# Performance work log

Hardware: AMD Instinct MI355X
Metric: run time of the kernel (lower is better)

## Reference

```python
import jax, jax.numpy as jnp
import numpy as np

N = 4096
C_IN = 256
C_OUT = 256
HEADS = 4
C_HEAD = C_OUT // HEADS
ALPHA = 0.2
NEG_FILL = -9e15


def setup_inputs() -> dict:
    key = jax.random.key(0)
    k1, k2, k3, k4 = jax.random.split(key, 4)
    node_feats = jax.random.normal(k1, (N, C_IN), dtype=jnp.float32)
    adj_matrix = jax.random.randint(k2, (1, N, N), 0, 2, dtype=jnp.int32)
    # xavier_uniform with gain=1.414
    lim_w = 1.414 * np.sqrt(6.0 / (C_IN + C_OUT))
    W = jax.random.uniform(k3, (C_OUT, C_IN), minval=-lim_w, maxval=lim_w, dtype=jnp.float32)
    b = jnp.zeros((C_OUT,), dtype=jnp.float32)
    lim_a = 1.414 * np.sqrt(6.0 / (HEADS + 2 * C_HEAD))
    a = jax.random.uniform(k4, (HEADS, 2 * C_HEAD), minval=-lim_a, maxval=lim_a, dtype=jnp.float32)
    return {"node_feats": node_feats, "adj_matrix": adj_matrix, "W": W, "b": b, "a": a}


def reference(node_feats, adj_matrix, W, b, a):
    # node_feats: [N, c_in] -> batch of 1, as in the torch 2D path
    h = (node_feats @ W.T + b).reshape(1, N, HEADS, C_HEAD)  # [1,N,H,c]
    a_src, a_dst = a[:, :C_HEAD], a[:, C_HEAD:]
    # attn logit for edge (i, j) = leakyrelu(a . [h_i, h_j])
    e_src = jnp.einsum('bnhc,hc->bnh', h, a_src)  # contribution of row node i
    e_dst = jnp.einsum('bnhc,hc->bnh', h, a_dst)  # contribution of col node j
    logits = jax.nn.leaky_relu(e_src[:, :, None, :] + e_dst[:, None, :, :], ALPHA)  # [1,N,N,H]
    mask = (adj_matrix == 1)[..., None]  # [1,N,N,1]
    attn = jnp.where(mask, logits, jnp.float32(NEG_FILL))
    probs = jax.nn.softmax(attn, axis=2)  # softmax over neighbors j
    out = jnp.einsum('bijh,bjhc->bihc', probs, h)  # [1,N,H,c]
    return out.reshape(1, N, HEADS * C_HEAD)  # concat heads
```

## Files before the change

kernel.cpp:

```cpp
#include <hip/hip_runtime.h>
#include <hip/hip_bf16.h>


#define NN 4096
#define LOG2E 1.4426950408889634f

typedef float f32x4 __attribute__((ext_vector_type(4)));
typedef int i32x4 __attribute__((ext_vector_type(4)));
typedef unsigned int u32x2 __attribute__((ext_vector_type(2)));
typedef unsigned int u32x4 __attribute__((ext_vector_type(4)));
typedef unsigned short u16x4 __attribute__((ext_vector_type(4)));
typedef unsigned short u16x8 __attribute__((ext_vector_type(8)));
typedef __bf16 bf16x8 __attribute__((ext_vector_type(8)));

__device__ __forceinline__ unsigned short f2bf_rne(float f) {
    unsigned int u = __builtin_bit_cast(unsigned int, f);
    u += 0x7fffu + ((u >> 16) & 1u);
    return (unsigned short)(u >> 16);
}

__device__ __forceinline__ bf16x8 ld_cvt8(const float* __restrict__ p) {
    f32x4 x = *(const f32x4*)p;
    f32x4 y = *(const f32x4*)(p + 4);
    u16x8 u;
    u[0] = f2bf_rne(x[0]); u[1] = f2bf_rne(x[1]); u[2] = f2bf_rne(x[2]); u[3] = f2bf_rne(x[3]);
    u[4] = f2bf_rne(y[0]); u[5] = f2bf_rne(y[1]); u[6] = f2bf_rne(y[2]); u[7] = f2bf_rne(y[3]);
    return __builtin_bit_cast(bf16x8, u);
}

__global__ __launch_bounds__(256) void k1_fused(const float* __restrict__ X,
                                                const float* __restrict__ W,
                                                const float* __restrict__ bias,
                                                const float* __restrict__ a,
                                                unsigned short* __restrict__ hB,
                                                float* __restrict__ esrc,
                                                float* __restrict__ edst) {
    const int lane = threadIdx.x & 63;
    const int hh   = threadIdx.x >> 6;
    const int row  = lane & 15;
    const int kg   = lane >> 4;
    const int rowbase = blockIdx.x * 16;

    f32x4 acc[4];
#pragma unroll
    for (int n = 0; n < 4; ++n) acc[n] = (f32x4)0.f;

#pragma unroll
    for (int kk = 0; kk < 8; ++kk) {
        const int kb = kk * 32 + kg * 8;
        bf16x8 a0 = ld_cvt8(X + (rowbase + row) * 256 + kb);
#pragma unroll
        for (int n = 0; n < 4; ++n) {
            bf16x8 bb = ld_cvt8(W + (hh * 64 + n * 16 + row) * 256 + kb);
            acc[n] = __builtin_amdgcn_mfma_f32_16x16x32_bf16(a0, bb, acc[n], 0, 0, 0);
        }
    }

    const int t   = rowbase >> 5;
    const int lp  = (((rowbase >> 4) & 1) * 2 + (kg >> 1)) * 16 + row;
    const int eoff = (kg & 1) * 4;
    unsigned short* hbb = hB + (hh * 128 + t) * 2048 + lp * 8 + eoff;

    float eS0 = 0.f, eS1 = 0.f, eS2 = 0.f, eS3 = 0.f;
    float eT0 = 0.f, eT1 = 0.f, eT2 = 0.f, eT3 = 0.f;
#pragma unroll
    for (int n = 0; n < 4; ++n) {
        const int col = hh * 64 + n * 16 + row;
        const float bv = bias[col];
        f32x4 hv;
        hv[0] = acc[n][0] + bv; hv[1] = acc[n][1] + bv;
        hv[2] = acc[n][2] + bv; hv[3] = acc[n][3] + bv;
        u16x4 us;
        us[0] = f2bf_rne(hv[0]); us[1] = f2bf_rne(hv[1]);
        us[2] = f2bf_rne(hv[2]); us[3] = f2bf_rne(hv[3]);
        *(u16x4*)(hbb + n * 512) = us;
        const float as_ = a[hh * 128 + n * 16 + row];
        const float ad_ = a[hh * 128 + 64 + n * 16 + row];
        eS0 += hv[0] * as_; eS1 += hv[1] * as_; eS2 += hv[2] * as_; eS3 += hv[3] * as_;
        eT0 += hv[0] * ad_; eT1 += hv[1] * ad_; eT2 += hv[2] * ad_; eT3 += hv[3] * ad_;
    }
#pragma unroll
    for (int d = 1; d < 16; d <<= 1) {
        eS0 += __shfl_xor(eS0, d); eS1 += __shfl_xor(eS1, d);
        eS2 += __shfl_xor(eS2, d); eS3 += __shfl_xor(eS3, d);
        eT0 += __shfl_xor(eT0, d); eT1 += __shfl_xor(eT1, d);
        eT2 += __shfl_xor(eT2, d); eT3 += __shfl_xor(eT3, d);
    }
    if (row == 0) {
        const int rb = hh * NN + rowbase + kg * 4;
        esrc[rb + 0] = eS0 * LOG2E; esrc[rb + 1] = eS1 * LOG2E;
        esrc[rb + 2] = eS2 * LOG2E; esrc[rb + 3] = eS3 * LOG2E;
        edst[rb + 0] = eT0 * LOG2E; edst[rb + 1] = eT1 * LOG2E;
        edst[rb + 2] = eT2 * LOG2E; edst[rb + 3] = eT3 * LOG2E;
    }
}

#define K3_MKP(AF, ES, M8) {                                                      \
    f32x4 s0v = E0 + (f32x4)(ES);                                                 \
    f32x4 s1v = E1 + (f32x4)(ES);                                                 \
    s0v = __builtin_elementwise_max(s0v, s0v * 0.2f);                             \
    s1v = __builtin_elementwise_max(s1v, s1v * 0.2f);                             \
    bf16x8 afv;                                                                   \
    afv[0] = (__bf16)__builtin_exp2f(s0v[0]);                                     \
    afv[1] = (__bf16)__builtin_exp2f(s0v[1]);                                     \
    afv[2] = (__bf16)__builtin_exp2f(s0v[2]);                                     \
    afv[3] = (__bf16)__builtin_exp2f(s0v[3]);                                     \
    afv[4] = (__bf16)__builtin_exp2f(s1v[0]);                                     \
    afv[5] = (__bf16)__builtin_exp2f(s1v[1]);                                     \
    afv[6] = (__bf16)__builtin_exp2f(s1v[2]);                                     \
    afv[7] = (__bf16)__builtin_exp2f(s1v[3]);                                     \
    u32x4 aw = __builtin_bit_cast(u32x4, afv);                                    \
    const u32x2 mk0 = mlut[(M8) & 15u];                                           \
    const u32x2 mk1 = mlut[((M8) >> 4) & 15u];                                    \
    aw[0] &= mk0[0]; aw[1] &= mk0[1];                                             \
    aw[2] &= mk1[0]; aw[3] &= mk1[1];                                             \
    AF = __builtin_bit_cast(bf16x8, aw);                                          \
}

__global__ __launch_bounds__(512, 4) void k3_flash(const int* __restrict__ adj,
                                                   const unsigned short* __restrict__ hB,
                                                   const float* __restrict__ esrc,
                                                   const float* __restrict__ edst,
                                                   float* __restrict__ out) {
    __shared__ float lacc[8][16][64];
    __shared__ float lls[8][16];
    __shared__ u32x2 mlut[16];

    const int lane = threadIdx.x & 63;
    const int q  = threadIdx.x >> 6;
    const int hh = blockIdx.x & 3;
    const int ib = blockIdx.x >> 2;
    const int i0 = ib * 32;
    const int row = lane & 15;
    const int kg  = lane >> 4;

    if (threadIdx.x < 16) {
        const unsigned n = threadIdx.x;
        u32x2 m;
        m[0] = ((n & 1u) ? 0xFFFFu : 0u) | ((n & 2u) ? 0xFFFF0000u : 0u);
        m[1] = ((n & 4u) ? 0xFFFFu : 0u) | ((n & 8u) ? 0xFFFF0000u : 0u);
        mlut[n] = m;
    }
    __syncthreads();

    const float es0 = esrc[hh * NN + i0 + row];
    const float es1 = esrc[hh * NN + i0 + 16 + row];
    const int* adj0 = adj + (i0 + row) * NN + q * 512 + kg * 8;
    const int* adj1 = adj0 + 16 * NN;
    const float* eD = edst + hh * NN + q * 512 + kg * 8;
    const unsigned short* hBp = hB + ((hh * 128 + q * 16) * 256 + lane) * 8;

    u16x8 ou;
    const unsigned short ov = (row == 0) ? (unsigned short)0x3F80 : (unsigned short)0;
#pragma unroll
    for (int e = 0; e < 8; ++e) ou[e] = ov;
    const bf16x8 bOnes = __builtin_bit_cast(bf16x8, ou);

    f32x4 aA0 = (f32x4)0.f, aA1 = (f32x4)0.f, aA2 = (f32x4)0.f,
          aA3 = (f32x4)0.f, aA4 = (f32x4)0.f;
    f32x4 aB0 = (f32x4)0.f, aB1 = (f32x4)0.f, aB2 = (f32x4)0.f,
          aB3 = (f32x4)0.f, aB4 = (f32x4)0.f;

    for (int td = 0; td < 4; ++td) {
        unsigned w0 = 0, w1 = 0;
#pragma unroll
        for (int ti = 0; ti < 4; ++ti) {
            const i32x4 pa0 = *(const i32x4*)(adj0 + td * 128 + ti * 32);
            const i32x4 pa1 = *(const i32x4*)(adj0 + td * 128 + ti * 32 + 4);
            const i32x4 pb0 = *(const i32x4*)(adj1 + td * 128 + ti * 32);
            const i32x4 pb1 = *(const i32x4*)(adj1 + td * 128 + ti * 32 + 4);
            unsigned b0 = 0, b1 = 0;
#pragma unroll
            for (int e = 0; e < 4; ++e) {
                b0 |= (unsigned)(pa0[e] & 1) << e;
                b0 |= (unsigned)(pa1[e] & 1) << (4 + e);
                b1 |= (unsigned)(pb0[e] & 1) << e;
                b1 |= (unsigned)(pb1[e] & 1) << (4 + e);
            }
            w0 |= b0 << (ti * 8);
            w1 |= b1 << (ti * 8);
        }

        const float* eDt = eD + td * 128;
        const unsigned short* hBt = hBp + td * 8192;
#pragma unroll
        for (int ti = 0; ti < 4; ++ti) {
            const f32x4 E0 = *(const f32x4*)(eDt + ti * 32);
            const f32x4 E1 = *(const f32x4*)(eDt + ti * 32 + 4);
            const u16x8 B0 = *(const u16x8*)(hBt + ti * 2048);
            const u16x8 B1 = *(const u16x8*)(hBt + ti * 2048 + 512);
            const u16x8 B2 = *(const u16x8*)(hBt + ti * 2048 + 1024);
            const u16x8 B3 = *(const u16x8*)(hBt + ti * 2048 + 1536);
            bf16x8 af0, af1;
            K3_MKP(af0, es0, (w0 >> (ti * 8)))
            K3_MKP(af1, es1, (w1 >> (ti * 8)))
            aA0 = __builtin_amdgcn_mfma_f32_16x16x32_bf16(af0, __builtin_bit_cast(bf16x8, B0), aA0, 0, 0, 0);
            aA1 = __builtin_amdgcn_mfma_f32_16x16x32_bf16(af0, __builtin_bit_cast(bf16x8, B1), aA1, 0, 0, 0);
            aA2 = __builtin_amdgcn_mfma_f32_16x16x32_bf16(af0, __builtin_bit_cast(bf16x8, B2), aA2, 0, 0, 0);
            aA3 = __builtin_amdgcn_mfma_f32_16x16x32_bf16(af0, __builtin_bit_cast(bf16x8, B3), aA3, 0, 0, 0);
            aA4 = __builtin_amdgcn_mfma_f32_16x16x32_bf16(af0, bOnes, aA4, 0, 0, 0);
            aB0 = __builtin_amdgcn_mfma_f32_16x16x32_bf16(af1, __builtin_bit_cast(bf16x8, B0), aB0, 0, 0, 0);
            aB1 = __builtin_amdgcn_mfma_f32_16x16x32_bf16(af1, __builtin_bit_cast(bf16x8, B1), aB1, 0, 0, 0);
            aB2 = __builtin_amdgcn_mfma_f32_16x16x32_bf16(af1, __builtin_bit_cast(bf16x8, B2), aB2, 0, 0, 0);
            aB3 = __builtin_amdgcn_mfma_f32_16x16x32_bf16(af1, __builtin_bit_cast(bf16x8, B3), aB3, 0, 0, 0);
            aB4 = __builtin_amdgcn_mfma_f32_16x16x32_bf16(af1, bOnes, aB4, 0, 0, 0);
        }
    }

#pragma unroll
    for (int n = 0; n < 4; ++n) {
        f32x4 an = (n == 0) ? aA0 : (n == 1) ? aA1 : (n == 2) ? aA2 : aA3;
#pragma unroll
        for (int r = 0; r < 4; ++r)
            lacc[q][kg * 4 + r][n * 16 + row] = an[r];
    }
    if (row == 0) {
#pragma unroll
        for (int r = 0; r < 4; ++r) lls[q][kg * 4 + r] = aA4[r];
    }
    __syncthreads();
    if (threadIdx.x < 256) {
        const int idx = threadIdx.x * 4;
        const int r2 = idx >> 6;
        const int c  = idx & 63;
        f32x4 v = (f32x4)0.f;
        float l = 0.f;
#pragma unroll
        for (int q2 = 0; q2 < 8; ++q2) {
            v += *(const f32x4*)&lacc[q2][r2][c];
            l += lls[q2][r2];
        }
        const float inv = 1.f / l;
        f32x4 o;
        o[0] = v[0] * inv; o[1] = v[1] * inv; o[2] = v[2] * inv; o[3] = v[3] * inv;
        *(f32x4*)(out + (i0 + r2) * 256 + hh * 64 + c) = o;
    }
    __syncthreads();

#pragma unroll
    for (int n = 0; n < 4; ++n) {
        f32x4 an = (n == 0) ? aB0 : (n == 1) ? aB1 : (n == 2) ? aB2 : aB3;
#pragma unroll
        for (int r = 0; r < 4; ++r)
            lacc[q][kg * 4 + r][n * 16 + row] = an[r];
    }
    if (row == 0) {
#pragma unroll
        for (int r = 0; r < 4; ++r) lls[q][kg * 4 + r] = aB4[r];
    }
    __syncthreads();
    if (threadIdx.x < 256) {
        const int idx = threadIdx.x * 4;
        const int r2 = idx >> 6;
        const int c  = idx & 63;
        f32x4 v = (f32x4)0.f;
        float l = 0.f;
#pragma unroll
        for (int q2 = 0; q2 < 8; ++q2) {
            v += *(const f32x4*)&lacc[q2][r2][c];
            l += lls[q2][r2];
        }
        const float inv = 1.f / l;
        f32x4 o;
        o[0] = v[0] * inv; o[1] = v[1] * inv; o[2] = v[2] * inv; o[3] = v[3] * inv;
        *(f32x4*)(out + (i0 + 16 + r2) * 256 + hh * 64 + c) = o;
    }
}

extern "C" void kernel_launch(void* const* d_in, const int* in_sizes, int n_in,
                              void* d_out, int out_size, void* d_ws, size_t ws_size,
                              hipStream_t stream) {
    const float* X    = (const float*)d_in[0];
    const int*   adj  = (const int*)d_in[1];
    const float* W    = (const float*)d_in[2];
    const float* bias = (const float*)d_in[3];
    const float* a    = (const float*)d_in[4];
    float* out = (float*)d_out;

    char* ws = (char*)d_ws;
    unsigned short* hB   = (unsigned short*)(ws);
    float*          esrc = (float*)(ws + (2 << 20));
    float*          edst = (float*)(ws + (2 << 20) + (64 << 10));

    k1_fused<<<256, 256, 0, stream>>>(X, W, bias, a, hB, esrc, edst);
    k3_flash<<<512, 512, 0, stream>>>(adj, hB, esrc, edst, out);
}
```

Measured before the change: 68.12 us.

## Stream adjacency through LDS with async triple-buffered loads and retile work split

The attention kernel now stages the int32 adjacency rows into shared memory with global_load_lds in a three-deep ring, waiting on vmcnt so the loads overlap the exp/MFMA work. The work split also changes: each block takes 64 rows of one head, each wave owns 16 rows and half the neighbor range, and the grid halves to 256 blocks. The final reduction is simpler because only two waves per row group are combined. In exchange, LDS use grows by 96 KB per block and occupancy is lowered to 2 blocks per CU, and each wave reuses its B fragments for only one row tile instead of two.

Result: faster. 66.34 us (-2.6%).

```diff
diff --git a/kernel.cpp b/kernel.cpp
--- a/kernel.cpp
+++ b/kernel.cpp
@@ -100,16 +100,15 @@
     f32x4 s1v = E1 + (f32x4)(ES);                                                 \
     s0v = __builtin_elementwise_max(s0v, s0v * 0.2f);                             \
     s1v = __builtin_elementwise_max(s1v, s1v * 0.2f);                             \
-    bf16x8 afv;                                                                   \
-    afv[0] = (__bf16)__builtin_exp2f(s0v[0]);                                     \
-    afv[1] = (__bf16)__builtin_exp2f(s0v[1]);                                     \
-    afv[2] = (__bf16)__builtin_exp2f(s0v[2]);                                     \
-    afv[3] = (__bf16)__builtin_exp2f(s0v[3]);                                     \
-    afv[4] = (__bf16)__builtin_exp2f(s1v[0]);                                     \
-    afv[5] = (__bf16)__builtin_exp2f(s1v[1]);                                     \
-    afv[6] = (__bf16)__builtin_exp2f(s1v[2]);                                     \
-    afv[7] = (__bf16)__builtin_exp2f(s1v[3]);                                     \
-    u32x4 aw = __builtin_bit_cast(u32x4, afv);                                    \
+    AF[0] = (__bf16)__builtin_exp2f(s0v[0]);                                      \
+    AF[1] = (__bf16)__builtin_exp2f(s0v[1]);                                      \
+    AF[2] = (__bf16)__builtin_exp2f(s0v[2]);                                      \
+    AF[3] = (__bf16)__builtin_exp2f(s0v[3]);                                      \
+    AF[4] = (__bf16)__builtin_exp2f(s1v[0]);                                      \
+    AF[5] = (__bf16)__builtin_exp2f(s1v[1]);                                      \
+    AF[6] = (__bf16)__builtin_exp2f(s1v[2]);                                      \
+    AF[7] = (__bf16)__builtin_exp2f(s1v[3]);                                      \
+    u32x4 aw = __builtin_bit_cast(u32x4, AF);                                     \
     const u32x2 mk0 = mlut[(M8) & 15u];                                           \
     const u32x2 mk1 = mlut[((M8) >> 4) & 15u];                                    \
     aw[0] &= mk0[0]; aw[1] &= mk0[1];                                             \
@@ -117,22 +116,64 @@
     AF = __builtin_bit_cast(bf16x8, aw);                                          \
 }
 
-__global__ __launch_bounds__(512, 4) void k3_flash(const int* __restrict__ adj,
+#define K3_STAGE(IT, BUF) {                                                       \
+    _Pragma("unroll")                                                             \
+    for (int k = 0; k < 4; ++k)                                                   \
+        __builtin_amdgcn_global_load_lds(                                         \
+            (const __attribute__((address_space(1))) void*)(gbase + (size_t)k * 16384 + (IT) * 64), \
+            (__attribute__((address_space(3))) void*)(&abuf[w][BUF][4 * k][0]),   \
+            16, 0, 0);                                                            \
+}
+
+#define K3_BODY(IT, BUF) {                                                        \
+    const unsigned int* ab = &abuf[w][BUF][0][0];                                 \
+    _Pragma("unroll")                                                             \
+    for (int lt = 0; lt < 2; ++lt) {                                              \
+        const int tl = (IT) * 2 + lt;                                             \
+        const int iloc = (lt * 32 + kg8) ^ rsw;                                   \
+        const u32x4 v0 = *(const u32x4*)(ab + row * 64 + iloc);                   \
+        const u32x4 v1 = *(const u32x4*)(ab + row * 64 + iloc + 4);               \
+        const f32x4 E0 = *(const f32x4*)(eD + tl * 32);                           \
+        const f32x4 E1 = *(const f32x4*)(eD + tl * 32 + 4);                       \
+        const u16x8 B0 = *(const u16x8*)(hBp + tl * 2048);                        \
+        const u16x8 B1 = *(const u16x8*)(hBp + tl * 2048 + 512);                  \
+        const u16x8 B2 = *(const u16x8*)(hBp + tl * 2048 + 1024);                 \
+        const u16x8 B3 = *(const u16x8*)(hBp + tl * 2048 + 1536);                 \
+        unsigned m8 = (v0[0] & 1u)        | ((v0[1] & 1u) << 1)                   \
+                    | ((v0[2] & 1u) << 2) | ((v0[3] & 1u) << 3)                   \
+                    | ((v1[0] & 1u) << 4) | ((v1[1] & 1u) << 5)                   \
+                    | ((v1[2] & 1u) << 6) | ((v1[3] & 1u) << 7);                  \
+        bf16x8 af;                                                                \
+        K3_MKP(af, es0, m8)                                                       \
+        a0 = __builtin_amdgcn_mfma_f32_16x16x32_bf16(af, __builtin_bit_cast(bf16x8, B0), a0, 0, 0, 0); \
+        a1 = __builtin_amdgcn_mfma_f32_16x16x32_bf16(af, __builtin_bit_cast(bf16x8, B1), a1, 0, 0, 0); \
+        a2 = __builtin_amdgcn_mfma_f32_16x16x32_bf16(af, __builtin_bit_cast(bf16x8, B2), a2, 0, 0, 0); \
+        a3 = __builtin_amdgcn_mfma_f32_16x16x32_bf16(af, __builtin_bit_cast(bf16x8, B3), a3, 0, 0, 0); \
+        a4 = __builtin_amdgcn_mfma_f32_16x16x32_bf16(af, bOnes, a4, 0, 0, 0);     \
+    }                                                                             \
+}
+
+__global__ __launch_bounds__(512, 2) void k3_flash(const int* __restrict__ adj,
                                                    const unsigned short* __restrict__ hB,
                                                    const float* __restrict__ esrc,
                                                    const float* __restrict__ edst,
                                                    float* __restrict__ out) {
+    __shared__ unsigned int abuf[8][3][16][64];
     __shared__ float lacc[8][16][64];
     __shared__ float lls[8][16];
     __shared__ u32x2 mlut[16];
 
     const int lane = threadIdx.x & 63;
-    const int q  = threadIdx.x >> 6;
-    const int hh = blockIdx.x & 3;
-    const int ib = blockIdx.x >> 2;
-    const int i0 = ib * 32;
+    const int w  = threadIdx.x >> 6;
+    const int rg = w >> 1;
+    const int jh = w & 1;
+    const int hh = blockIdx.x >> 6;
+    const int ib = blockIdx.x & 63;
+    const int i0 = ib * 64;
     const int row = lane & 15;
     const int kg  = lane >> 4;
+    const int kg8 = kg * 8;
+    const int rsw = (row & 3) << 3;
 
     if (threadIdx.x < 16) {
         const unsigned n = threadIdx.x;
@@ -143,12 +184,14 @@
     }
     __syncthreads();
 
-    const float es0 = esrc[hh * NN + i0 + row];
-    const float es1 = esrc[hh * NN + i0 + 16 + row];
-    const int* adj0 = adj + (i0 + row) * NN + q * 512 + kg * 8;
-    const int* adj1 = adj0 + 16 * NN;
-    const float* eD = edst + hh * NN + q * 512 + kg * 8;
-    const unsigned short* hBp = hB + ((hh * 128 + q * 16) * 256 + lane) * 8;
+    const int lr4  = lane >> 4;
+    const int gloc = (4 * (lane & 15)) ^ (lr4 << 3);
+    const unsigned int* gbase = (const unsigned int*)adj
+        + (size_t)(i0 + rg * 16 + lr4) * NN + jh * 2048 + gloc;
+
+    const float es0 = esrc[hh * NN + i0 + rg * 16 + row];
+    const float* eD = edst + hh * NN + jh * 2048 + kg8;
+    const unsigned short* hBp = hB + (size_t)((hh * 128 + jh * 64) * 256 + lane) * 8;
 
     u16x8 ou;
     const unsigned short ov = (row == 0) ? (unsigned short)0x3F80 : (unsigned short)0;
@@ -156,114 +199,54 @@
     for (int e = 0; e < 8; ++e) ou[e] = ov;
     const bf16x8 bOnes = __builtin_bit_cast(bf16x8, ou);
 
-    f32x4 aA0 = (f32x4)0.f, aA1 = (f32x4)0.f, aA2 = (f32x4)0.f,
-          aA3 = (f32x4)0.f, aA4 = (f32x4)0.f;
-    f32x4 aB0 = (f32x4)0.f, aB1 = (f32x4)0.f, aB2 = (f32x4)0.f,
-          aB3 = (f32x4)0.f, aB4 = (f32x4)0.f;
-
-    for (int td = 0; td < 4; ++td) {
-        unsigned w0 = 0, w1 = 0;
-#pragma unroll
-        for (int ti = 0; ti < 4; ++ti) {
-            const i32x4 pa0 = *(const i32x4*)(adj0 + td * 128 + ti * 32);
-            const i32x4 pa1 = *(const i32x4*)(adj0 + td * 128 + ti * 32 + 4);
-            const i32x4 pb0 = *(const i32x4*)(adj1 + td * 128 + ti * 32);
-            const i32x4 pb1 = *(const i32x4*)(adj1 + td * 128 + ti * 32 + 4);
-            unsigned b0 = 0, b1 = 0;
-#pragma unroll
-            for (int e = 0; e < 4; ++e) {
-                b0 |= (unsigned)(pa0[e] & 1) << e;
-                b0 |= (unsigned)(pa1[e] & 1) << (4 + e);
-                b1 |= (unsigned)(pb0[e] & 1) << e;
-                b1 |= (unsigned)(pb1[e] & 1) << (4 + e);
-            }
-            w0 |= b0 << (ti * 8);
-            w1 |= b1 << (ti * 8);
+    f32x4 a0 = (f32x4)0.f, a1 = (f32x4)0.f, a2 = (f32x4)0.f,
+          a3 = (f32x4)0.f, a4 = (f32x4)0.f;
+
+    K3_STAGE(0, 0)
+    K3_STAGE(1, 1)
+    for (int it = 0; it < 31; ++it) {
+        asm volatile("s_waitcnt vmcnt(4)" ::: "memory");
+        __builtin_amdgcn_sched_barrier(0);
+        const int bf = it % 3;
+        K3_BODY(it, bf)
+        if (it < 30) {
+            const int sb = (it + 2) % 3;
+            K3_STAGE(it + 2, sb)
         }
-
-        const float* eDt = eD + td * 128;
-        const unsigned short* hBt = hBp + td * 8192;
-#pragma unroll
-        for (int ti = 0; ti < 4; ++ti) {
-            const f32x4 E0 = *(const f32x4*)(eDt + ti * 32);
-            const f32x4 E1 = *(const f32x4*)(eDt + ti * 32 + 4);
-            const u16x8 B0 = *(const u16x8*)(hBt + ti * 2048);
-            const u16x8 B1 = *(const u16x8*)(hBt + ti * 2048 + 512);
-            const u16x8 B2 = *(const u16x8*)(hBt + ti * 2048 + 1024);
-            const u16x8 B3 = *(const u16x8*)(hBt + ti * 2048 + 1536);
-            bf16x8 af0, af1;
-            K3_MKP(af0, es0, (w0 >> (ti * 8)))
-            K3_MKP(af1, es1, (w1 >> (ti * 8)))
-            aA0 = __builtin_amdgcn_mfma_f32_16x16x32_bf16(af0, __builtin_bit_cast(bf16x8, B0), aA0, 0, 0, 0);
-            aA1 = __builtin_amdgcn_mfma_f32_16x16x32_bf16(af0, __builtin_bit_cast(bf16x8, B1), aA1, 0, 0, 0);
-            aA2 = __builtin_amdgcn_mfma_f32_16x16x32_bf16(af0, __builtin_bit_cast(bf16x8, B2), aA2, 0, 0, 0);
-            aA3 = __builtin_amdgcn_mfma_f32_16x16x32_bf16(af0, __builtin_bit_cast(bf16x8, B3), aA3, 0, 0, 0);
-            aA4 = __builtin_amdgcn_mfma_f32_16x16x32_bf16(af0, bOnes, aA4, 0, 0, 0);
-            aB0 = __builtin_amdgcn_mfma_f32_16x16x32_bf16(af1, __builtin_bit_cast(bf16x8, B0), aB0, 0, 0, 0);
-            aB1 = __builtin_amdgcn_mfma_f32_16x16x32_bf16(af1, __builtin_bit_cast(bf16x8, B1), aB1, 0, 0, 0);
-            aB2 = __builtin_amdgcn_mfma_f32_16x16x32_bf16(af1, __builtin_bit_cast(bf16x8, B2), aB2, 0, 0, 0);
-            aB3 = __builtin_amdgcn_mfma_f32_16x16x32_bf16(af1, __builtin_bit_cast(bf16x8, B3), aB3, 0, 0, 0);
-            aB4 = __builtin_amdgcn_mfma_f32_16x16x32_bf16(af1, bOnes, aB4, 0, 0, 0);
-        }
-    }
+    }
+    asm volatile("s_waitcnt vmcnt(0)" ::: "memory");
+    __builtin_amdgcn_sched_barrier(0);
+    K3_BODY(31, 1)
 
 #pragma unroll
     for (int n = 0; n < 4; ++n) {
-        f32x4 an = (n == 0) ? aA0 : (n == 1) ? aA1 : (n == 2) ? aA2 : aA3;
+        f32x4 an = (n == 0) ? a0 : (n == 1) ? a1 : (n == 2) ? a2 : a3;
 #pragma unroll
         for (int r = 0; r < 4; ++r)
-            lacc[q][kg * 4 + r][n * 16 + row] = an[r];
+            lacc[w][kg * 4 + r][n * 16 + row] = an[r];
     }
     if (row == 0) {
 #pragma unroll
-        for (int r = 0; r < 4; ++r) lls[q][kg * 4 + r] = aA4[r];
+        for (int r = 0; r < 4; ++r) lls[w][kg * 4 + r] = a4[r];
     }
     __syncthreads();
-    if (threadIdx.x < 256) {
-        const int idx = threadIdx.x * 4;
-        const int r2 = idx >> 6;
-        const int c  = idx & 63;
-        f32x4 v = (f32x4)0.f;
-        float l = 0.f;
-#pragma unroll
-        for (int q2 = 0; q2 < 8; ++q2) {
-            v += *(const f32x4*)&lacc[q2][r2][c];
-            l += lls[q2][r2];
-        }
-        const float inv = 1.f / l;
-        f32x4 o;
-        o[0] = v[0] * inv; o[1] = v[1] * inv; o[2] = v[2] * inv; o[3] = v[3] * inv;
-        *(f32x4*)(out + (i0 + r2) * 256 + hh * 64 + c) = o;
-    }
-    __syncthreads();
-
-#pragma unroll
-    for (int n = 0; n < 4; ++n) {
-        f32x4 an = (n == 0) ? aB0 : (n == 1) ? aB1 : (n == 2) ? aB2 : aB3;
-#pragma unroll
-        for (int r = 0; r < 4; ++r)
-            lacc[q][kg * 4 + r][n * 16 + row] = an[r];
-    }
-    if (row == 0) {
-#pragma unroll
-        for (int r = 0; r < 4; ++r) lls[q][kg * 4 + r] = aB4[r];
-    }
-    __syncthreads();
-    if (threadIdx.x < 256) {
-        const int idx = threadIdx.x * 4;
-        const int r2 = idx >> 6;
-        const int c  = idx & 63;
-        f32x4 v = (f32x4)0.f;
-        float l = 0.f;
-#pragma unroll
-        for (int q2 = 0; q2 < 8; ++q2) {
-            v += *(const f32x4*)&lacc[q2][r2][c];
-            l += lls[q2][r2];
-        }
-        const float inv = 1.f / l;
-        f32x4 o;
-        o[0] = v[0] * inv; o[1] = v[1] * inv; o[2] = v[2] * inv; o[3] = v[3] * inv;
-        *(f32x4*)(out + (i0 + 16 + r2) * 256 + hh * 64 + c) = o;
+
+    {
+        const int rg2 = threadIdx.x >> 7;
+        const int r2  = (threadIdx.x >> 3) & 15;
+        const int c8  = (threadIdx.x & 7) * 8;
+        const int wA = rg2 * 2, wB = rg2 * 2 + 1;
+        f32x4 v0 = *(const f32x4*)&lacc[wA][r2][c8];
+        f32x4 v1 = *(const f32x4*)&lacc[wA][r2][c8 + 4];
+        v0 += *(const f32x4*)&lacc[wB][r2][c8];
+        v1 += *(const f32x4*)&lacc[wB][r2][c8 + 4];
+        const float inv = 1.f / (lls[wA][r2] + lls[wB][r2]);
+        f32x4 o0, o1;
+        o0[0] = v0[0] * inv; o0[1] = v0[1] * inv; o0[2] = v0[2] * inv; o0[3] = v0[3] * inv;
+        o1[0] = v1[0] * inv; o1[1] = v1[1] * inv; o1[2] = v1[2] * inv; o1[3] = v1[3] * inv;
+        float* op = out + (size_t)(i0 + rg2 * 16 + r2) * 256 + hh * 64 + c8;
+        *(f32x4*)op = o0;
+        *(f32x4*)(op + 4) = o1;
     }
 }
 
@@ -283,5 +266,5 @@
     float*          edst = (float*)(ws + (2 << 20) + (64 << 10));
 
     k1_fused<<<256, 256, 0, stream>>>(X, W, bias, a, hB, esrc, edst);
-    k3_flash<<<512, 512, 0, stream>>>(adj, hB, esrc, edst, out);
-}
+    k3_flash<<<256, 512, 0, stream>>>(adj, hB, esrc, edst, out);
+}
```

## Process all heads per block to read adjacency once, with nontemporal prefetch

Applied to the files above, without the earlier changes.

Each block now handles 16 rows across all four heads instead of 32 rows for one head. The adjacency mask is therefore read once per row rather than once per head, which removes the dominant redundant traffic of the 64MB int32 matrix. Adjacency loads are nontemporal and prefetched one tile ahead. In exchange the block count drops to 256 and each thread holds 20 accumulators, with launch bounds relaxed to 2 blocks per CU. This raises register pressure and lowers occupancy, and the epilogue now runs four reduction rounds with barriers.

Result: slower. 72.98 us, median of 2 (+7.1%).

```diff
diff --git a/kernel.cpp b/kernel.cpp
--- a/kernel.cpp
+++ b/kernel.cpp
@@ -95,29 +95,7 @@
     }
 }
 
-#define K3_MKP(AF, ES, M8) {                                                      \
-    f32x4 s0v = E0 + (f32x4)(ES);                                                 \
-    f32x4 s1v = E1 + (f32x4)(ES);                                                 \
-    s0v = __builtin_elementwise_max(s0v, s0v * 0.2f);                             \
-    s1v = __builtin_elementwise_max(s1v, s1v * 0.2f);                             \
-    bf16x8 afv;                                                                   \
-    afv[0] = (__bf16)__builtin_exp2f(s0v[0]);                                     \
-    afv[1] = (__bf16)__builtin_exp2f(s0v[1]);                                     \
-    afv[2] = (__bf16)__builtin_exp2f(s0v[2]);                                     \
-    afv[3] = (__bf16)__builtin_exp2f(s0v[3]);                                     \
-    afv[4] = (__bf16)__builtin_exp2f(s1v[0]);                                     \
-    afv[5] = (__bf16)__builtin_exp2f(s1v[1]);                                     \
-    afv[6] = (__bf16)__builtin_exp2f(s1v[2]);                                     \
-    afv[7] = (__bf16)__builtin_exp2f(s1v[3]);                                     \
-    u32x4 aw = __builtin_bit_cast(u32x4, afv);                                    \
-    const u32x2 mk0 = mlut[(M8) & 15u];                                           \
-    const u32x2 mk1 = mlut[((M8) >> 4) & 15u];                                    \
-    aw[0] &= mk0[0]; aw[1] &= mk0[1];                                             \
-    aw[2] &= mk1[0]; aw[3] &= mk1[1];                                             \
-    AF = __builtin_bit_cast(bf16x8, aw);                                          \
-}
-
-__global__ __launch_bounds__(512, 4) void k3_flash(const int* __restrict__ adj,
+__global__ __launch_bounds__(512, 2) void k3_fused(const int* __restrict__ adj,
                                                    const unsigned short* __restrict__ hB,
                                                    const float* __restrict__ esrc,
                                                    const float* __restrict__ edst,
@@ -128,11 +106,10 @@
 
     const int lane = threadIdx.x & 63;
     const int q  = threadIdx.x >> 6;
-    const int hh = blockIdx.x & 3;
-    const int ib = blockIdx.x >> 2;
-    const int i0 = ib * 32;
+    const int i0 = blockIdx.x * 16;
     const int row = lane & 15;
     const int kg  = lane >> 4;
+    const int kg8 = kg * 8;
 
     if (threadIdx.x < 16) {
         const unsigned n = threadIdx.x;
@@ -143,12 +120,19 @@
     }
     __syncthreads();
 
-    const float es0 = esrc[hh * NN + i0 + row];
-    const float es1 = esrc[hh * NN + i0 + 16 + row];
-    const int* adj0 = adj + (i0 + row) * NN + q * 512 + kg * 8;
-    const int* adj1 = adj0 + 16 * NN;
-    const float* eD = edst + hh * NN + q * 512 + kg * 8;
-    const unsigned short* hBp = hB + ((hh * 128 + q * 16) * 256 + lane) * 8;
+    float es[4];
+#pragma unroll
+    for (int h = 0; h < 4; ++h) es[h] = esrc[h * NN + i0 + row];
+
+    const unsigned int* adjp = (const unsigned int*)adj
+        + (size_t)(i0 + row) * NN + q * 512 + kg8;
+    const float* eD[4];
+    const unsigned short* hBp[4];
+#pragma unroll
+    for (int h = 0; h < 4; ++h) {
+        eD[h]  = edst + h * NN + q * 512 + kg8;
+        hBp[h] = hB + (size_t)((h * 128 + q * 16) * 256 + lane) * 8;
+    }
 
     u16x8 ou;
     const unsigned short ov = (row == 0) ? (unsigned short)0x3F80 : (unsigned short)0;
@@ -156,114 +140,92 @@
     for (int e = 0; e < 8; ++e) ou[e] = ov;
     const bf16x8 bOnes = __builtin_bit_cast(bf16x8, ou);
 
-    f32x4 aA0 = (f32x4)0.f, aA1 = (f32x4)0.f, aA2 = (f32x4)0.f,
-          aA3 = (f32x4)0.f, aA4 = (f32x4)0.f;
-    f32x4 aB0 = (f32x4)0.f, aB1 = (f32x4)0.f, aB2 = (f32x4)0.f,
-          aB3 = (f32x4)0.f, aB4 = (f32x4)0.f;
-
-    for (int td = 0; td < 4; ++td) {
-        unsigned w0 = 0, w1 = 0;
-#pragma unroll
-        for (int ti = 0; ti < 4; ++ti) {
-            const i32x4 pa0 = *(const i32x4*)(adj0 + td * 128 + ti * 32);
-            const i32x4 pa1 = *(const i32x4*)(adj0 + td * 128 + ti * 32 + 4);
-            const i32x4 pb0 = *(const i32x4*)(adj1 + td * 128 + ti * 32);
-            const i32x4 pb1 = *(const i32x4*)(adj1 + td * 128 + ti * 32 + 4);
-            unsigned b0 = 0, b1 = 0;
-#pragma unroll
-            for (int e = 0; e < 4; ++e) {
-                b0 |= (unsigned)(pa0[e] & 1) << e;
-                b0 |= (unsigned)(pa1[e] & 1) << (4 + e);
-                b1 |= (unsigned)(pb0[e] & 1) << e;
-                b1 |= (unsigned)(pb1[e] & 1) << (4 + e);
+    f32x4 acc[4][5];
+#pragma unroll
+    for (int h = 0; h < 4; ++h)
+#pragma unroll
+        for (int n = 0; n < 5; ++n) acc[h][n] = (f32x4)0.f;
+
+    u32x4 c0 = __builtin_nontemporal_load((const u32x4*)(adjp));
+    u32x4 c1 = __builtin_nontemporal_load((const u32x4*)(adjp + 4));
+
+    for (int tl = 0; tl < 16; ++tl) {
+        u32x4 n0, n1;
+        if (tl < 15) {
+            n0 = __builtin_nontemporal_load((const u32x4*)(adjp + (tl + 1) * 32));
+            n1 = __builtin_nontemporal_load((const u32x4*)(adjp + (tl + 1) * 32 + 4));
+        }
+        const unsigned m8 = (c0[0] & 1u)        | ((c0[1] & 1u) << 1)
+                          | ((c0[2] & 1u) << 2) | ((c0[3] & 1u) << 3)
+                          | ((c1[0] & 1u) << 4) | ((c1[1] & 1u) << 5)
+                          | ((c1[2] & 1u) << 6) | ((c1[3] & 1u) << 7);
+        const u32x2 mk0 = mlut[m8 & 15u];
+        const u32x2 mk1 = mlut[(m8 >> 4) & 15u];
+
+#pragma unroll
+        for (int h = 0; h < 4; ++h) {
+            const f32x4 E0 = *(const f32x4*)(eD[h] + tl * 32);
+            const f32x4 E1 = *(const f32x4*)(eD[h] + tl * 32 + 4);
+            const u16x8 B0 = *(const u16x8*)(hBp[h] + tl * 2048);
+            const u16x8 B1 = *(const u16x8*)(hBp[h] + tl * 2048 + 512);
+            const u16x8 B2 = *(const u16x8*)(hBp[h] + tl * 2048 + 1024);
+            const u16x8 B3 = *(const u16x8*)(hBp[h] + tl * 2048 + 1536);
+            f32x4 s0v = E0 + (f32x4)(es[h]);
+            f32x4 s1v = E1 + (f32x4)(es[h]);
+            s0v = __builtin_elementwise_max(s0v, s0v * 0.2f);
+            s1v = __builtin_elementwise_max(s1v, s1v * 0.2f);
+            bf16x8 af;
+            af[0] = (__bf16)__builtin_exp2f(s0v[0]);
+            af[1] = (__bf16)__builtin_exp2f(s0v[1]);
+            af[2] = (__bf16)__builtin_exp2f(s0v[2]);
+            af[3] = (__bf16)__builtin_exp2f(s0v[3]);
+            af[4] = (__bf16)__builtin_exp2f(s1v[0]);
+            af[5] = (__bf16)__builtin_exp2f(s1v[1]);
+            af[6] = (__bf16)__builtin_exp2f(s1v[2]);
+            af[7] = (__bf16)__builtin_exp2f(s1v[3]);
+            u32x4 aw = __builtin_bit_cast(u32x4, af);
+            aw[0] &= mk0[0]; aw[1] &= mk0[1];
+            aw[2] &= mk1[0]; aw[3] &= mk1[1];
+            af = __builtin_bit_cast(bf16x8, aw);
+            acc[h][0] = __builtin_amdgcn_mfma_f32_16x16x32_bf16(af, __builtin_bit_cast(bf16x8, B0), acc[h][0], 0, 0, 0);
+            acc[h][1] = __builtin_amdgcn_mfma_f32_16x16x32_bf16(af, __builtin_bit_cast(bf16x8, B1), acc[h][1], 0, 0, 0);
+            acc[h][2] = __builtin_amdgcn_mfma_f32_16x16x32_bf16(af, __builtin_bit_cast(bf16x8, B2), acc[h][2], 0, 0, 0);
+            acc[h][3] = __builtin_amdgcn_mfma_f32_16x16x32_bf16(af, __builtin_bit_cast(bf16x8, B3), acc[h][3], 0, 0, 0);
+            acc[h][4] = __builtin_amdgcn_mfma_f32_16x16x32_bf16(af, bOnes, acc[h][4], 0, 0, 0);
+        }
+        c0 = n0; c1 = n1;
+    }
+
+#pragma unroll
+    for (int h = 0; h < 4; ++h) {
+#pragma unroll
+        for (int n = 0; n < 4; ++n) {
+#pragma unroll
+            for (int r = 0; r < 4; ++r)
+                lacc[q][kg * 4 + r][n * 16 + row] = acc[h][n][r];
+        }
+        if (row == 0) {
+#pragma unroll
+            for (int r = 0; r < 4; ++r) lls[q][kg * 4 + r] = acc[h][4][r];
+        }
+        __syncthreads();
+        if (threadIdx.x < 256) {
+            const int idx = threadIdx.x * 4;
+            const int r2 = idx >> 6;
+            const int c  = idx & 63;
+            f32x4 v = (f32x4)0.f;
+            float l = 0.f;
+#pragma unroll
+            for (int q2 = 0; q2 < 8; ++q2) {
+                v += *(const f32x4*)&lacc[q2][r2][c];
+                l += lls[q2][r2];
             }
-            w0 |= b0 << (ti * 8);
-            w1 |= b1 << (ti * 8);
-        }
-
-        const float* eDt = eD + td * 128;
-        const unsigned short* hBt = hBp + td * 8192;
-#pragma unroll
-        for (int ti = 0; ti < 4; ++ti) {
-            const f32x4 E0 = *(const f32x4*)(eDt + ti * 32);
-            const f32x4 E1 = *(const f32x4*)(eDt + ti * 32 + 4);
-            const u16x8 B0 = *(const u16x8*)(hBt + ti * 2048);
-            const u16x8 B1 = *(const u16x8*)(hBt + ti * 2048 + 512);
-            const u16x8 B2 = *(const u16x8*)(hBt + ti * 2048 + 1024);
-            const u16x8 B3 = *(const u16x8*)(hBt + ti * 2048 + 1536);
-            bf16x8 af0, af1;
-            K3_MKP(af0, es0, (w0 >> (ti * 8)))
-            K3_MKP(af1, es1, (w1 >> (ti * 8)))
-            aA0 = __builtin_amdgcn_mfma_f32_16x16x32_bf16(af0, __builtin_bit_cast(bf16x8, B0), aA0, 0, 0, 0);
-            aA1 = __builtin_amdgcn_mfma_f32_16x16x32_bf16(af0, __builtin_bit_cast(bf16x8, B1), aA1, 0, 0, 0);
-            aA2 = __builtin_amdgcn_mfma_f32_16x16x32_bf16(af0, __builtin_bit_cast(bf16x8, B2), aA2, 0, 0, 0);
-            aA3 = __builtin_amdgcn_mfma_f32_16x16x32_bf16(af0, __builtin_bit_cast(bf16x8, B3), aA3, 0, 0, 0);
-            aA4 = __builtin_amdgcn_mfma_f32_16x16x32_bf16(af0, bOnes, aA4, 0, 0, 0);
-            aB0 = __builtin_amdgcn_mfma_f32_16x16x32_bf16(af1, __builtin_bit_cast(bf16x8, B0), aB0, 0, 0, 0);
-            aB1 = __builtin_amdgcn_mfma_f32_16x16x32_bf16(af1, __builtin_bit_cast(bf16x8, B1), aB1, 0, 0, 0);
-            aB2 = __builtin_amdgcn_mfma_f32_16x16x32_bf16(af1, __builtin_bit_cast(bf16x8, B2), aB2, 0, 0, 0);
-            aB3 = __builtin_amdgcn_mfma_f32_16x16x32_bf16(af1, __builtin_bit_cast(bf16x8, B3), aB3, 0, 0, 0);
-            aB4 = __builtin_amdgcn_mfma_f32_16x16x32_bf16(af1, bOnes, aB4, 0, 0, 0);
-        }
-    }
-
-#pragma unroll
-    for (int n = 0; n < 4; ++n) {
-        f32x4 an = (n == 0) ? aA0 : (n == 1) ? aA1 : (n == 2) ? aA2 : aA3;
-#pragma unroll
-        for (int r = 0; r < 4; ++r)
-            lacc[q][kg * 4 + r][n * 16 + row] = an[r];
-    }
-    if (row == 0) {
-#pragma unroll
-        for (int r = 0; r < 4; ++r) lls[q][kg * 4 + r] = aA4[r];
-    }
-    __syncthreads();
-    if (threadIdx.x < 256) {
-        const int idx = threadIdx.x * 4;
-        const int r2 = idx >> 6;
-        const int c  = idx & 63;
-        f32x4 v = (f32x4)0.f;
-        float l = 0.f;
-#pragma unroll
-        for (int q2 = 0; q2 < 8; ++q2) {
-            v += *(const f32x4*)&lacc[q2][r2][c];
-            l += lls[q2][r2];
-        }
-        const float inv = 1.f / l;
-        f32x4 o;
-        o[0] = v[0] * inv; o[1] = v[1] * inv; o[2] = v[2] * inv; o[3] = v[3] * inv;
-        *(f32x4*)(out + (i0 + r2) * 256 + hh * 64 + c) = o;
-    }
-    __syncthreads();
-
-#pragma unroll
-    for (int n = 0; n < 4; ++n) {
-        f32x4 an = (n == 0) ? aB0 : (n == 1) ? aB1 : (n == 2) ? aB2 : aB3;
-#pragma unroll
-        for (int r = 0; r < 4; ++r)
-            lacc[q][kg * 4 + r][n * 16 + row] = an[r];
-    }
-    if (row == 0) {
-#pragma unroll
-        for (int r = 0; r < 4; ++r) lls[q][kg * 4 + r] = aB4[r];
-    }
-    __syncthreads();
-    if (threadIdx.x < 256) {
-        const int idx = threadIdx.x * 4;
-        const int r2 = idx >> 6;
-        const int c  = idx & 63;
-        f32x4 v = (f32x4)0.f;
-        float l = 0.f;
-#pragma unroll
-        for (int q2 = 0; q2 < 8; ++q2) {
-            v += *(const f32x4*)&lacc[q2][r2][c];
-            l += lls[q2][r2];
-        }
-        const float inv = 1.f / l;
-        f32x4 o;
-        o[0] = v[0] * inv; o[1] = v[1] * inv; o[2] = v[2] * inv; o[3] = v[3] * inv;
-        *(f32x4*)(out + (i0 + 16 + r2) * 256 + hh * 64 + c) = o;
+            const float inv = 1.f / l;
+            f32x4 o;
+            o[0] = v[0] * inv; o[1] = v[1] * inv; o[2] = v[2] * inv; o[3] = v[3] * inv;
+            *(f32x4*)(out + (i0 + r2) * 256 + h * 64 + c) = o;
+        }
+        __syncthreads();
     }
 }
 
@@ -283,5 +245,5 @@
     float*          edst = (float*)(ws + (2 << 20) + (64 << 10));
 
     k1_fused<<<256, 256, 0, stream>>>(X, W, bias, a, hB, esrc, edst);
-    k3_flash<<<512, 512, 0, stream>>>(adj, hB, esrc, edst, out);
-}
+    k3_fused<<<256, 512, 0, stream>>>(adj, hB, esrc, edst, out);
+}
```
